# Kernel tuning notes

Hardware: AMD Instinct MI355X
Metric: run time of the kernel (lower is better)

## Reference

```python
import jax, jax.numpy as jnp
import numpy as np

B, N, M, C = 4, 4096, 4096, 256
IMG_W, IMG_H = 1242.0, 376.0  # KITTI-like image extents for keypoint coords


def setup_inputs() -> dict:
    key = jax.random.key(0)
    ks = jax.random.split(key, 12)
    s = 1.0 / np.sqrt(C)
    scale_uv = jnp.array([IMG_W, IMG_H], dtype=jnp.float32)
    return {
        "nodes_L": jax.random.normal(ks[0], (B, N, C), jnp.float32),
        "nodes_R": jax.random.normal(ks[1], (B, M, C), jnp.float32),
        "kpts_L": jax.random.uniform(ks[2], (B, N, 2), jnp.float32) * scale_uv,
        "kpts_R": jax.random.uniform(ks[3], (B, M, 2), jnp.float32) * scale_uv,
        "Wq": jax.random.normal(ks[4], (C, C), jnp.float32) * s,
        "bq": jnp.zeros((C,), jnp.float32),
        "Wk": jax.random.normal(ks[5], (C, C), jnp.float32) * s,
        "bk": jnp.zeros((C,), jnp.float32),
        "Wv": jax.random.normal(ks[6], (C, C), jnp.float32) * s,
        "bv": jnp.zeros((C,), jnp.float32),
        "Wm": jax.random.normal(ks[7], (C, C), jnp.float32) * s,
        "bm": jnp.zeros((C,), jnp.float32),
    }


def reference(nodes_L, nodes_R, kpts_L, kpts_R, Wq, bq, Wk, bk, Wv, bv, Wm, bm):
    dim = nodes_L.shape[-1]
    # torch.nn.Linear: y = x @ W.T + b  (W is [out, in])
    Q = jnp.einsum('bnc,dc->bnd', nodes_L, Wq) + bq  # [B,N,C]
    K = jnp.einsum('bmc,dc->bmd', nodes_R, Wk) + bk  # [B,M,C]
    V = jnp.einsum('bmc,dc->bmd', nodes_R, Wv) + bv  # [B,M,C]

    # Epipolar geometric mask from keypoint coordinates
    dist_v = jnp.abs(kpts_L[:, :, 1:2] - kpts_R[:, None, :, 1])  # [B,N,M]
    dist_u = kpts_L[:, :, 0:1] - kpts_R[:, None, :, 0]           # [B,N,M]
    mask = (dist_v < 3.0) & (dist_u > 0) & (dist_u < 192)

    attn = jnp.einsum('bnd,bmd->bnm', Q, K) / (dim ** 0.5)       # [B,N,M]
    attn = jnp.where(mask, attn, jnp.float32(-1e9))
    attn_weights = jax.nn.softmax(attn, axis=-1)                 # [B,N,M]

    matched_features = jnp.einsum('bnm,bmd->bnd', attn_weights, V)
    init_disparity = jnp.sum(attn_weights * dist_u, axis=-1, keepdims=True)  # [B,N,1]
    confidence = jnp.any(mask, axis=-1, keepdims=True).astype(jnp.float32)   # [B,N,1]
    out = jnp.einsum('bnd,cd->bnc', matched_features, Wm) + bm   # [B,N,C]
    return (out, init_disparity, confidence, attn_weights)
```

## Files before the change

### kernel.cpp

```cpp
#include <hip/hip_runtime.h>
#include <stdint.h>

#define CAP 192

typedef __attribute__((ext_vector_type(4))) float f32x4;
typedef __attribute__((ext_vector_type(8))) short bf16x8;

__device__ __forceinline__ float bf2f(ushort u) {
  return __uint_as_float(((unsigned)u) << 16);
}
__device__ __forceinline__ ushort f2bf(float f) {
  unsigned u = __float_as_uint(f);
  return (ushort)((u + 0x7fffu + ((u >> 16) & 1u)) >> 16);
}
__device__ __forceinline__ float wredsum(float v) {
#pragma unroll
  for (int o = 32; o; o >>= 1) v += __shfl_xor(v, o);
  return v;
}

__global__ __launch_bounds__(256) void prep(const float* __restrict__ nodesR,
                                            const float* __restrict__ kptsR,
                                            float* __restrict__ S16,
                                            float* __restrict__ sumU16,
                                            float* __restrict__ attn) {
  int t = threadIdx.x;
  if (blockIdx.x < 64) {
    int b = blockIdx.x >> 4, ch = blockIdx.x & 15;
    int c4 = (t & 63) * 4;
    int r0 = b * 4096 + ch * 256 + (t >> 6);
    float4 acc = {0.f, 0.f, 0.f, 0.f};
    for (int k = 0; k < 64; ++k) {
      float4 v = *(const float4*)(nodesR + (size_t)(r0 + k * 4) * 256 + c4);
      acc.x += v.x; acc.y += v.y; acc.z += v.z; acc.w += v.w;
    }
    __shared__ float4 red[256];
    red[t] = acc;
    float u = kptsR[(size_t)(b * 4096 + ch * 256 + t) * 2];
    u = wredsum(u);
    __shared__ float ured[4];
    if ((t & 63) == 0) ured[t >> 6] = u;
    __syncthreads();
    if (t < 64) {
      float4 x = red[t], y = red[t + 64], z = red[t + 128], w = red[t + 192];
      float4 s = { x.x + y.x + z.x + w.x, x.y + y.y + z.y + w.y,
                   x.z + y.z + z.z + w.z, x.w + y.w + z.w + w.w };
      *(float4*)(S16 + (size_t)(b * 16 + ch) * 256 + t * 4) = s;
    }
    if (t == 0) sumU16[b * 16 + ch] = ured[0] + ured[1] + ured[2] + ured[3];
  }
  f32x4 z = {0.f, 0.f, 0.f, 0.f};
  f32x4* dst = (f32x4*)attn;
  int g = blockIdx.x * 256 + t;
#pragma unroll
  for (int i = 0; i < 32; ++i)
    __builtin_nontemporal_store(z, dst + (size_t)g + (size_t)i * 524288);
}

template <bool A_BF16, typename OutT>
__device__ __forceinline__ void gemm_body(const void* __restrict__ Av,
                                          const float* __restrict__ Wf,
                                          const float* __restrict__ bias,
                                          OutT* __restrict__ Y, int blk,
                                          ushort* As, ushort* Bs) {
  int tid = threadIdx.x;
  int lane = tid & 63, wid = tid >> 6;
  int bm = blk >> 1, bn = blk & 1;
  int r0 = bm * 128, c0 = bn * 128;
  int wr = wid >> 1, wc = wid & 1;
  f32x4 acc[4][4] = {};
  for (int k0 = 0; k0 < 256; k0 += 32) {
    __syncthreads();
#pragma unroll
    for (int p = 0; p < 2; ++p) {
      int u = p * 2048 + tid * 8;
      int row = u >> 5, col = u & 31;
      if constexpr (A_BF16) {
        *(bf16x8*)&As[u] =
            *(const bf16x8*)((const ushort*)Av + (size_t)(r0 + row) * 256 + k0 + col);
      } else {
        const float* Af = (const float*)Av;
        float4 lo = *(const float4*)(Af + (size_t)(r0 + row) * 256 + k0 + col);
        float4 hi = *(const float4*)(Af + (size_t)(r0 + row) * 256 + k0 + col + 4);
        ushort4 o0 = { f2bf(lo.x), f2bf(lo.y), f2bf(lo.z), f2bf(lo.w) };
        ushort4 o1 = { f2bf(hi.x), f2bf(hi.y), f2bf(hi.z), f2bf(hi.w) };
        *(ushort4*)&As[u] = o0;
        *(ushort4*)&As[u + 4] = o1;
      }
      {
        float4 lo = *(const float4*)(Wf + (size_t)(c0 + row) * 256 + k0 + col);
        float4 hi = *(const float4*)(Wf + (size_t)(c0 + row) * 256 + k0 + col + 4);
        ushort4 o0 = { f2bf(lo.x), f2bf(lo.y), f2bf(lo.z), f2bf(lo.w) };
        ushort4 o1 = { f2bf(hi.x), f2bf(hi.y), f2bf(hi.z), f2bf(hi.w) };
        *(ushort4*)&Bs[u] = o0;
        *(ushort4*)&Bs[u + 4] = o1;
      }
    }
    __syncthreads();
    bf16x8 af[4], bfr[4];
    int rsel = lane & 15, ksel = (lane >> 4) * 8;
#pragma unroll
    for (int m = 0; m < 4; ++m)
      af[m] = *(bf16x8*)&As[(wr * 64 + m * 16 + rsel) * 32 + ksel];
#pragma unroll
    for (int n = 0; n < 4; ++n)
      bfr[n] = *(bf16x8*)&Bs[(wc * 64 + n * 16 + rsel) * 32 + ksel];
#pragma unroll
    for (int m = 0; m < 4; ++m)
#pragma unroll
      for (int n = 0; n < 4; ++n)
        acc[m][n] = __builtin_amdgcn_mfma_f32_16x16x32_bf16(af[m], bfr[n], acc[m][n], 0, 0, 0);
  }
  int rbase = r0 + wr * 64 + ((lane >> 4) * 4);
  int cbase = c0 + wc * 64 + (lane & 15);
#pragma unroll
  for (int n = 0; n < 4; ++n) {
    float bv = bias[cbase + n * 16];
#pragma unroll
    for (int m = 0; m < 4; ++m) {
#pragma unroll
      for (int j = 0; j < 4; ++j) {
        float v = acc[m][n][j] + bv;
        size_t idx = (size_t)(rbase + m * 16 + j) * 256 + (cbase + n * 16);
        if constexpr (sizeof(OutT) == 2) Y[idx] = (OutT)f2bf(v);
        else Y[idx] = (OutT)v;
      }
    }
  }
}

__global__ __launch_bounds__(256, 2) void gemm3p(
    const float* __restrict__ nodesL, const float* __restrict__ nodesR,
    const float* __restrict__ Wq, const float* __restrict__ Wk,
    const float* __restrict__ Wv, const float* __restrict__ bq,
    const float* __restrict__ bk, const float* __restrict__ bv,
    ushort* __restrict__ Qb, ushort* __restrict__ Kb, ushort* __restrict__ Vb,
    const float* __restrict__ S16, const float* __restrict__ sumU16,
    ushort* __restrict__ meanVb, float* __restrict__ meanU) {
  __shared__ __align__(16) ushort As[128 * 32];
  __shared__ __align__(16) ushort Bs[128 * 32];
  if (blockIdx.x == 768) {
    int c = threadIdx.x;
    float* sf = (float*)As;
    for (int b = 0; b < 4; ++b) {
      float a0 = 0.f;
      for (int ch = 0; ch < 16; ++ch) a0 += S16[(size_t)(b * 16 + ch) * 256 + c];
      sf[c] = a0;
      __syncthreads();
      float acc = 0.f;
      for (int k = 0; k < 256; k += 4) {
        float4 w = *(const float4*)(Wv + (size_t)c * 256 + k);
        acc += sf[k] * w.x + sf[k + 1] * w.y + sf[k + 2] * w.z + sf[k + 3] * w.w;
      }
      float mv = acc * (1.f / 4096.f) + bv[c];
      meanVb[b * 256 + c] = f2bf(mv);
      if (c == 0) {
        float su = 0.f;
        for (int ch = 0; ch < 16; ++ch) su += sumU16[b * 16 + ch];
        meanU[b] = su * (1.f / 4096.f);
      }
      __syncthreads();
    }
    return;
  }
  int which = blockIdx.x >> 8;
  int blk = blockIdx.x & 255;
  const float* A = (which == 0) ? nodesL : nodesR;
  const float* W = (which == 0) ? Wq : (which == 1) ? Wk : Wv;
  const float* bias = (which == 0) ? bq : (which == 1) ? bk : bv;
  ushort* Y = (which == 0) ? Qb : (which == 1) ? Kb : Vb;
  gemm_body<false, ushort>(A, W, bias, Y, blk, As, Bs);
}

__global__ __launch_bounds__(256, 2) void gemm_out(const ushort* __restrict__ A,
                                                   const float* __restrict__ Wm,
                                                   const float* __restrict__ bias,
                                                   float* __restrict__ Y) {
  __shared__ __align__(16) ushort As[128 * 32];
  __shared__ __align__(16) ushort Bs[128 * 32];
  gemm_body<true, float>(A, Wm, bias, Y, blockIdx.x, As, Bs);
}

__global__ __launch_bounds__(512, 2) void attn_fused(
    const float* __restrict__ kptsL, const float* __restrict__ kptsR,
    const ushort* __restrict__ Qb, const ushort* __restrict__ Kb,
    const ushort* __restrict__ Vb, const float* __restrict__ meanU,
    const ushort* __restrict__ meanVb, float* __restrict__ disp_out,
    float* __restrict__ conf_out, ushort* __restrict__ matched,
    float* __restrict__ attn) {
  __shared__ float2 kR[4096];
  __shared__ int bufM[8][CAP];
  __shared__ float bufD[8][CAP];
  __shared__ float bufS[8][CAP];
  int tid = threadIdx.x, lane = tid & 63, wid = tid >> 6;
  int b = blockIdx.x >> 9;
  int n = ((blockIdx.x & 511) << 3) + wid;
  int row = (b << 12) + n;
  int bb = b << 12;
  float* rowp = attn + (size_t)row * 4096;

  const float2* kRsrc = (const float2*)kptsR + (size_t)bb;
  for (int i = tid; i < 4096; i += 512) kR[i] = kRsrc[i];
  __syncthreads();
  float2 kL = ((const float2*)kptsL)[(size_t)row];
  ushort4 qv = *(const ushort4*)(Qb + (size_t)row * 256 + lane * 4);
  float q0 = bf2f(qv.x), q1 = bf2f(qv.y), q2 = bf2f(qv.z), q3 = bf2f(qv.w);

  unsigned long long lmask = (1ull << lane) - 1ull;
  int cnt = 0;
#pragma unroll 4
  for (int m0 = 0; m0 < 4096; m0 += 64) {
    float2 kr = kR[m0 + lane];
    float dv = fabsf(kL.y - kr.y);
    float du = kL.x - kr.x;
    bool hit = (dv < 3.0f) && (du > 0.0f) && (du < 192.0f);
    unsigned long long bal = __ballot(hit);
    int pos = cnt + (int)__popcll(bal & lmask);
    if (hit && pos < CAP) { bufM[wid][pos] = m0 + lane; bufD[wid][pos] = du; }
    cnt += (int)__popcll(bal);
  }
  if (cnt > CAP) cnt = CAP;

  float conf, disp;
  if (cnt == 0) {
    conf = 0.f;
    disp = kL.x - meanU[b];
    ushort4 st = *(const ushort4*)(meanVb + b * 256 + lane * 4);
    *(ushort4*)(matched + (size_t)row * 256 + lane * 4) = st;
    const float fill = 1.f / 4096.f;
    f32x4 fv = { fill, fill, fill, fill };
    f32x4* dst = (f32x4*)rowp;
#pragma unroll
    for (int j = 0; j < 16; ++j)
      __builtin_nontemporal_store(fv, dst + j * 64 + lane);
  } else {
    float mx = -1e30f;
    int i = 0;
    for (; i + 3 < cnt; i += 4) {
      int m0_ = bufM[wid][i], m1_ = bufM[wid][i + 1];
      int m2_ = bufM[wid][i + 2], m3_ = bufM[wid][i + 3];
      ushort4 k0 = *(const ushort4*)(Kb + ((size_t)(bb + m0_)) * 256 + lane * 4);
      ushort4 k1 = *(const ushort4*)(Kb + ((size_t)(bb + m1_)) * 256 + lane * 4);
      ushort4 k2 = *(const ushort4*)(Kb + ((size_t)(bb + m2_)) * 256 + lane * 4);
      ushort4 k3 = *(const ushort4*)(Kb + ((size_t)(bb + m3_)) * 256 + lane * 4);
      float p0 = q0 * bf2f(k0.x) + q1 * bf2f(k0.y) + q2 * bf2f(k0.z) + q3 * bf2f(k0.w);
      float p1 = q0 * bf2f(k1.x) + q1 * bf2f(k1.y) + q2 * bf2f(k1.z) + q3 * bf2f(k1.w);
      float p2 = q0 * bf2f(k2.x) + q1 * bf2f(k2.y) + q2 * bf2f(k2.z) + q3 * bf2f(k2.w);
      float p3 = q0 * bf2f(k3.x) + q1 * bf2f(k3.y) + q2 * bf2f(k3.z) + q3 * bf2f(k3.w);
#pragma unroll
      for (int o = 32; o; o >>= 1) {
        p0 += __shfl_xor(p0, o);
        p1 += __shfl_xor(p1, o);
        p2 += __shfl_xor(p2, o);
        p3 += __shfl_xor(p3, o);
      }
      float s0 = p0 * 0.0625f, s1 = p1 * 0.0625f;
      float s2 = p2 * 0.0625f, s3 = p3 * 0.0625f;
      if (lane == 0) {
        bufS[wid][i] = s0; bufS[wid][i + 1] = s1;
        bufS[wid][i + 2] = s2; bufS[wid][i + 3] = s3;
      }
      mx = fmaxf(mx, fmaxf(fmaxf(s0, s1), fmaxf(s2, s3)));
    }
    for (; i < cnt; ++i) {
      int ma = bufM[wid][i];
      ushort4 ka = *(const ushort4*)(Kb + ((size_t)(bb + ma)) * 256 + lane * 4);
      float pa = q0 * bf2f(ka.x) + q1 * bf2f(ka.y) + q2 * bf2f(ka.z) + q3 * bf2f(ka.w);
      pa = wredsum(pa);
      float sa = pa * 0.0625f;
      if (lane == 0) bufS[wid][i] = sa;
      mx = fmaxf(mx, sa);
    }
    float psum = 0.f, pdisp = 0.f;
    for (int k = lane; k < cnt; k += 64) {
      float e = expf(bufS[wid][k] - mx);
      bufS[wid][k] = e;
      psum += e;
      pdisp += e * bufD[wid][k];
    }
    psum = wredsum(psum);
    pdisp = wredsum(pdisp);
    float inv = 1.f / psum;
    disp = pdisp * inv;
    conf = 1.f;
    for (int k = lane; k < cnt; k += 64) bufS[wid][k] *= inv;
    float a0 = 0.f, a1 = 0.f, a2 = 0.f, a3 = 0.f;
    i = 0;
    for (; i + 3 < cnt; i += 4) {
      float w0 = bufS[wid][i], w1 = bufS[wid][i + 1];
      float w2 = bufS[wid][i + 2], w3 = bufS[wid][i + 3];
      int m0_ = bufM[wid][i], m1_ = bufM[wid][i + 1];
      int m2_ = bufM[wid][i + 2], m3_ = bufM[wid][i + 3];
      ushort4 v0 = *(const ushort4*)(Vb + ((size_t)(bb + m0_)) * 256 + lane * 4);
      ushort4 v1 = *(const ushort4*)(Vb + ((size_t)(bb + m1_)) * 256 + lane * 4);
      ushort4 v2 = *(const ushort4*)(Vb + ((size_t)(bb + m2_)) * 256 + lane * 4);
      ushort4 v3 = *(const ushort4*)(Vb + ((size_t)(bb + m3_)) * 256 + lane * 4);
      a0 += w0 * bf2f(v0.x) + w1 * bf2f(v1.x) + w2 * bf2f(v2.x) + w3 * bf2f(v3.x);
      a1 += w0 * bf2f(v0.y) + w1 * bf2f(v1.y) + w2 * bf2f(v2.y) + w3 * bf2f(v3.y);
      a2 += w0 * bf2f(v0.z) + w1 * bf2f(v1.z) + w2 * bf2f(v2.z) + w3 * bf2f(v3.z);
      a3 += w0 * bf2f(v0.w) + w1 * bf2f(v1.w) + w2 * bf2f(v2.w) + w3 * bf2f(v3.w);
    }
    for (; i < cnt; ++i) {
      float wa = bufS[wid][i];
      int ma = bufM[wid][i];
      ushort4 va = *(const ushort4*)(Vb + ((size_t)(bb + ma)) * 256 + lane * 4);
      a0 += wa * bf2f(va.x); a1 += wa * bf2f(va.y);
      a2 += wa * bf2f(va.z); a3 += wa * bf2f(va.w);
    }
    ushort4 st = { f2bf(a0), f2bf(a1), f2bf(a2), f2bf(a3) };
    *(ushort4*)(matched + (size_t)row * 256 + lane * 4) = st;
    for (int k = lane; k < cnt; k += 64)
      rowp[bufM[wid][k]] = bufS[wid][k];
  }
  if (lane == 0) { disp_out[row] = disp; conf_out[row] = conf; }
}

extern "C" void kernel_launch(void* const* d_in, const int* in_sizes, int n_in,
                              void* d_out, int out_size, void* d_ws, size_t ws_size,
                              hipStream_t stream) {
  const float* nodes_L = (const float*)d_in[0];
  const float* nodes_R = (const float*)d_in[1];
  const float* kpts_L = (const float*)d_in[2];
  const float* kpts_R = (const float*)d_in[3];
  const float* Wq = (const float*)d_in[4];
  const float* bq = (const float*)d_in[5];
  const float* Wk = (const float*)d_in[6];
  const float* bk = (const float*)d_in[7];
  const float* Wv = (const float*)d_in[8];
  const float* bv = (const float*)d_in[9];
  const float* Wm = (const float*)d_in[10];
  const float* bm = (const float*)d_in[11];

  float* out = (float*)d_out;
  float* disp = out + 4194304;
  float* conf = disp + 16384;
  float* attn = conf + 16384;

  char* ws = (char*)d_ws;
  ushort* Qb = (ushort*)(ws + 0);
  ushort* Kb = (ushort*)(ws + 8388608);
  ushort* Vb = (ushort*)(ws + 16777216);
  ushort* matched = (ushort*)(ws + 25165824);
  float* S16 = (float*)(ws + 33554432);
  float* sumU16 = (float*)(ws + 33620224);
  float* meanU = (float*)(ws + 33620480);
  ushort* meanVb = (ushort*)(ws + 33620544);

  prep<<<2048, 256, 0, stream>>>(nodes_R, kpts_R, S16, sumU16, attn);
  gemm3p<<<769, 256, 0, stream>>>(nodes_L, nodes_R, Wq, Wk, Wv, bq, bk, bv,
                                  Qb, Kb, Vb, S16, sumU16, meanVb, meanU);
  attn_fused<<<2048, 512, 0, stream>>>(kpts_L, kpts_R, Qb, Kb, Vb, meanU, meanVb,
                                       disp, conf, matched, attn);
  gemm_out<<<256, 256, 0, stream>>>(matched, Wm, bm, out);
}
```

Before: 474.4 us.

## Fuse all stages into one persistent cooperative kernel with grid syncs

Replaces the four separate launches (prep, QKV GEMM, attention, output GEMM) with a single cooperative kernel of 1024 blocks that uses grid-wide syncs between phases. The prep reduction and attention zero-fill move into the first phase, and each attention block now handles 16 rows with 4 rows per wave. The precomputed mean-V is replaced by an on-demand computation in rows with no epipolar match. The match buffer CAP shrinks from 192 to 128. This removes launch gaps and inter-kernel idle tails, at the cost of lower parallelism in the attention phase, grid-sync overhead, and a possible correctness change if a row has more than 128 matches.

Measured after the change: 791.8 us. +66.9%, slower.

```diff
diff --git a/kernel.cpp b/kernel.cpp
--- a/kernel.cpp
+++ b/kernel.cpp
@@ -1,7 +1,10 @@
 #include <hip/hip_runtime.h>
+#include <hip/hip_cooperative_groups.h>
 #include <stdint.h>
 
-#define CAP 192
+namespace cg = cooperative_groups;
+
+#define CAP 128
 
 typedef __attribute__((ext_vector_type(4))) float f32x4;
 typedef __attribute__((ext_vector_type(8))) short bf16x8;
@@ -17,44 +20,6 @@
 #pragma unroll
   for (int o = 32; o; o >>= 1) v += __shfl_xor(v, o);
   return v;
-}
-
-__global__ __launch_bounds__(256) void prep(const float* __restrict__ nodesR,
-                                            const float* __restrict__ kptsR,
-                                            float* __restrict__ S16,
-                                            float* __restrict__ sumU16,
-                                            float* __restrict__ attn) {
-  int t = threadIdx.x;
-  if (blockIdx.x < 64) {
-    int b = blockIdx.x >> 4, ch = blockIdx.x & 15;
-    int c4 = (t & 63) * 4;
-    int r0 = b * 4096 + ch * 256 + (t >> 6);
-    float4 acc = {0.f, 0.f, 0.f, 0.f};
-    for (int k = 0; k < 64; ++k) {
-      float4 v = *(const float4*)(nodesR + (size_t)(r0 + k * 4) * 256 + c4);
-      acc.x += v.x; acc.y += v.y; acc.z += v.z; acc.w += v.w;
-    }
-    __shared__ float4 red[256];
-    red[t] = acc;
-    float u = kptsR[(size_t)(b * 4096 + ch * 256 + t) * 2];
-    u = wredsum(u);
-    __shared__ float ured[4];
-    if ((t & 63) == 0) ured[t >> 6] = u;
-    __syncthreads();
-    if (t < 64) {
-      float4 x = red[t], y = red[t + 64], z = red[t + 128], w = red[t + 192];
-      float4 s = { x.x + y.x + z.x + w.x, x.y + y.y + z.y + w.y,
-                   x.z + y.z + z.z + w.z, x.w + y.w + z.w + w.w };
-      *(float4*)(S16 + (size_t)(b * 16 + ch) * 256 + t * 4) = s;
-    }
-    if (t == 0) sumU16[b * 16 + ch] = ured[0] + ured[1] + ured[2] + ured[3];
-  }
-  f32x4 z = {0.f, 0.f, 0.f, 0.f};
-  f32x4* dst = (f32x4*)attn;
-  int g = blockIdx.x * 256 + t;
-#pragma unroll
-  for (int i = 0; i < 32; ++i)
-    __builtin_nontemporal_store(z, dst + (size_t)g + (size_t)i * 524288);
 }
 
 template <bool A_BF16, typename OutT>
@@ -129,190 +94,238 @@
   }
 }
 
-__global__ __launch_bounds__(256, 2) void gemm3p(
+__device__ __forceinline__ void phase1_body(
     const float* __restrict__ nodesL, const float* __restrict__ nodesR,
-    const float* __restrict__ Wq, const float* __restrict__ Wk,
-    const float* __restrict__ Wv, const float* __restrict__ bq,
-    const float* __restrict__ bk, const float* __restrict__ bv,
+    const float* __restrict__ kptsR,
+    const float* __restrict__ Wq, const float* __restrict__ bq,
+    const float* __restrict__ Wk, const float* __restrict__ bk,
+    const float* __restrict__ Wv, const float* __restrict__ bv,
     ushort* __restrict__ Qb, ushort* __restrict__ Kb, ushort* __restrict__ Vb,
-    const float* __restrict__ S16, const float* __restrict__ sumU16,
-    ushort* __restrict__ meanVb, float* __restrict__ meanU) {
-  __shared__ __align__(16) ushort As[128 * 32];
-  __shared__ __align__(16) ushort Bs[128 * 32];
-  if (blockIdx.x == 768) {
-    int c = threadIdx.x;
-    float* sf = (float*)As;
-    for (int b = 0; b < 4; ++b) {
-      float a0 = 0.f;
-      for (int ch = 0; ch < 16; ++ch) a0 += S16[(size_t)(b * 16 + ch) * 256 + c];
-      sf[c] = a0;
-      __syncthreads();
-      float acc = 0.f;
-      for (int k = 0; k < 256; k += 4) {
-        float4 w = *(const float4*)(Wv + (size_t)c * 256 + k);
-        acc += sf[k] * w.x + sf[k + 1] * w.y + sf[k + 2] * w.z + sf[k + 3] * w.w;
-      }
-      float mv = acc * (1.f / 4096.f) + bv[c];
-      meanVb[b * 256 + c] = f2bf(mv);
-      if (c == 0) {
-        float su = 0.f;
-        for (int ch = 0; ch < 16; ++ch) su += sumU16[b * 16 + ch];
-        meanU[b] = su * (1.f / 4096.f);
-      }
-      __syncthreads();
-    }
-    return;
-  }
-  int which = blockIdx.x >> 8;
-  int blk = blockIdx.x & 255;
-  const float* A = (which == 0) ? nodesL : nodesR;
-  const float* W = (which == 0) ? Wq : (which == 1) ? Wk : Wv;
-  const float* bias = (which == 0) ? bq : (which == 1) ? bk : bv;
-  ushort* Y = (which == 0) ? Qb : (which == 1) ? Kb : Vb;
-  gemm_body<false, ushort>(A, W, bias, Y, blk, As, Bs);
-}
-
-__global__ __launch_bounds__(256, 2) void gemm_out(const ushort* __restrict__ A,
-                                                   const float* __restrict__ Wm,
-                                                   const float* __restrict__ bias,
-                                                   float* __restrict__ Y) {
-  __shared__ __align__(16) ushort As[128 * 32];
-  __shared__ __align__(16) ushort Bs[128 * 32];
-  gemm_body<true, float>(A, Wm, bias, Y, blockIdx.x, As, Bs);
-}
-
-__global__ __launch_bounds__(512, 2) void attn_fused(
+    float* __restrict__ S16, float* __restrict__ sumU16,
+    float* __restrict__ attn, char* smraw) {
+  int bid = blockIdx.x, tid = threadIdx.x;
+  ushort* As = (ushort*)smraw;
+  ushort* Bs = (ushort*)(smraw + 8192);
+  if (bid < 768) {
+    int which = bid >> 8, blk = bid & 255;
+    const float* A = (which == 0) ? nodesL : nodesR;
+    const float* W = (which == 0) ? Wq : (which == 1) ? Wk : Wv;
+    const float* bias = (which == 0) ? bq : (which == 1) ? bk : bv;
+    ushort* Y = (which == 0) ? Qb : (which == 1) ? Kb : Vb;
+    gemm_body<false, ushort>(A, W, bias, Y, blk, As, Bs);
+  } else if (bid < 832) {
+    int j = bid - 768;
+    int b = j >> 4, ch = j & 15;
+    int c4 = (tid & 63) * 4;
+    int r0 = b * 4096 + ch * 256 + (tid >> 6);
+    float4 acc = {0.f, 0.f, 0.f, 0.f};
+    for (int k = 0; k < 64; ++k) {
+      float4 v = *(const float4*)(nodesR + (size_t)(r0 + k * 4) * 256 + c4);
+      acc.x += v.x; acc.y += v.y; acc.z += v.z; acc.w += v.w;
+    }
+    float4* red = (float4*)As;
+    float* ured = (float*)Bs;
+    red[tid] = acc;
+    float u = kptsR[(size_t)(b * 4096 + ch * 256 + tid) * 2];
+    u = wredsum(u);
+    if ((tid & 63) == 0) ured[tid >> 6] = u;
+    __syncthreads();
+    if (tid < 64) {
+      float4 x = red[tid], y = red[tid + 64], z = red[tid + 128], w = red[tid + 192];
+      float4 s = { x.x + y.x + z.x + w.x, x.y + y.y + z.y + w.y,
+                   x.z + y.z + z.z + w.z, x.w + y.w + z.w + w.w };
+      *(float4*)(S16 + (size_t)(b * 16 + ch) * 256 + tid * 4) = s;
+    }
+    if (tid == 0) sumU16[b * 16 + ch] = ured[0] + ured[1] + ured[2] + ured[3];
+  }
+  f32x4 z = {0.f, 0.f, 0.f, 0.f};
+  f32x4* dst = (f32x4*)attn;
+  int g = bid * 256 + tid;
+#pragma unroll
+  for (int i = 0; i < 64; ++i)
+    __builtin_nontemporal_store(z, dst + (size_t)g + (size_t)i * 262144);
+}
+
+__device__ __forceinline__ void phase2_body(
     const float* __restrict__ kptsL, const float* __restrict__ kptsR,
     const ushort* __restrict__ Qb, const ushort* __restrict__ Kb,
-    const ushort* __restrict__ Vb, const float* __restrict__ meanU,
-    const ushort* __restrict__ meanVb, float* __restrict__ disp_out,
+    const ushort* __restrict__ Vb, const float* __restrict__ Wv,
+    const float* __restrict__ bv, const float* __restrict__ S16,
+    const float* __restrict__ sumU16, float* __restrict__ disp_out,
     float* __restrict__ conf_out, ushort* __restrict__ matched,
-    float* __restrict__ attn) {
-  __shared__ float2 kR[4096];
-  __shared__ int bufM[8][CAP];
-  __shared__ float bufD[8][CAP];
-  __shared__ float bufS[8][CAP];
-  int tid = threadIdx.x, lane = tid & 63, wid = tid >> 6;
-  int b = blockIdx.x >> 9;
-  int n = ((blockIdx.x & 511) << 3) + wid;
-  int row = (b << 12) + n;
+    float* __restrict__ attn, char* smraw) {
+  float2* kR = (float2*)smraw;
+  int   (*bufM)[CAP] = (int(*)[CAP])(smraw + 32768);
+  float (*bufD)[CAP] = (float(*)[CAP])(smraw + 34816);
+  float (*bufS)[CAP] = (float(*)[CAP])(smraw + 36864);
+  int bid = blockIdx.x, tid = threadIdx.x;
+  int lane = tid & 63, wid = tid >> 6;
+  int b = bid >> 8;
   int bb = b << 12;
-  float* rowp = attn + (size_t)row * 4096;
-
   const float2* kRsrc = (const float2*)kptsR + (size_t)bb;
-  for (int i = tid; i < 4096; i += 512) kR[i] = kRsrc[i];
+  for (int i = tid; i < 4096; i += 256) kR[i] = kRsrc[i];
   __syncthreads();
-  float2 kL = ((const float2*)kptsL)[(size_t)row];
-  ushort4 qv = *(const ushort4*)(Qb + (size_t)row * 256 + lane * 4);
-  float q0 = bf2f(qv.x), q1 = bf2f(qv.y), q2 = bf2f(qv.z), q3 = bf2f(qv.w);
-
   unsigned long long lmask = (1ull << lane) - 1ull;
-  int cnt = 0;
+
+  for (int r = 0; r < 4; ++r) {
+    int row = bid * 16 + wid * 4 + r;
+    float* rowp = attn + (size_t)row * 4096;
+    float2 kL = ((const float2*)kptsL)[(size_t)row];
+    ushort4 qv = *(const ushort4*)(Qb + (size_t)row * 256 + lane * 4);
+    float q0 = bf2f(qv.x), q1 = bf2f(qv.y), q2 = bf2f(qv.z), q3 = bf2f(qv.w);
+
+    int cnt = 0;
 #pragma unroll 4
-  for (int m0 = 0; m0 < 4096; m0 += 64) {
-    float2 kr = kR[m0 + lane];
-    float dv = fabsf(kL.y - kr.y);
-    float du = kL.x - kr.x;
-    bool hit = (dv < 3.0f) && (du > 0.0f) && (du < 192.0f);
-    unsigned long long bal = __ballot(hit);
-    int pos = cnt + (int)__popcll(bal & lmask);
-    if (hit && pos < CAP) { bufM[wid][pos] = m0 + lane; bufD[wid][pos] = du; }
-    cnt += (int)__popcll(bal);
-  }
-  if (cnt > CAP) cnt = CAP;
-
-  float conf, disp;
-  if (cnt == 0) {
-    conf = 0.f;
-    disp = kL.x - meanU[b];
-    ushort4 st = *(const ushort4*)(meanVb + b * 256 + lane * 4);
-    *(ushort4*)(matched + (size_t)row * 256 + lane * 4) = st;
-    const float fill = 1.f / 4096.f;
-    f32x4 fv = { fill, fill, fill, fill };
-    f32x4* dst = (f32x4*)rowp;
-#pragma unroll
-    for (int j = 0; j < 16; ++j)
-      __builtin_nontemporal_store(fv, dst + j * 64 + lane);
-  } else {
-    float mx = -1e30f;
-    int i = 0;
-    for (; i + 3 < cnt; i += 4) {
-      int m0_ = bufM[wid][i], m1_ = bufM[wid][i + 1];
-      int m2_ = bufM[wid][i + 2], m3_ = bufM[wid][i + 3];
-      ushort4 k0 = *(const ushort4*)(Kb + ((size_t)(bb + m0_)) * 256 + lane * 4);
-      ushort4 k1 = *(const ushort4*)(Kb + ((size_t)(bb + m1_)) * 256 + lane * 4);
-      ushort4 k2 = *(const ushort4*)(Kb + ((size_t)(bb + m2_)) * 256 + lane * 4);
-      ushort4 k3 = *(const ushort4*)(Kb + ((size_t)(bb + m3_)) * 256 + lane * 4);
-      float p0 = q0 * bf2f(k0.x) + q1 * bf2f(k0.y) + q2 * bf2f(k0.z) + q3 * bf2f(k0.w);
-      float p1 = q0 * bf2f(k1.x) + q1 * bf2f(k1.y) + q2 * bf2f(k1.z) + q3 * bf2f(k1.w);
-      float p2 = q0 * bf2f(k2.x) + q1 * bf2f(k2.y) + q2 * bf2f(k2.z) + q3 * bf2f(k2.w);
-      float p3 = q0 * bf2f(k3.x) + q1 * bf2f(k3.y) + q2 * bf2f(k3.z) + q3 * bf2f(k3.w);
-#pragma unroll
-      for (int o = 32; o; o >>= 1) {
-        p0 += __shfl_xor(p0, o);
-        p1 += __shfl_xor(p1, o);
-        p2 += __shfl_xor(p2, o);
-        p3 += __shfl_xor(p3, o);
-      }
-      float s0 = p0 * 0.0625f, s1 = p1 * 0.0625f;
-      float s2 = p2 * 0.0625f, s3 = p3 * 0.0625f;
-      if (lane == 0) {
-        bufS[wid][i] = s0; bufS[wid][i + 1] = s1;
-        bufS[wid][i + 2] = s2; bufS[wid][i + 3] = s3;
-      }
-      mx = fmaxf(mx, fmaxf(fmaxf(s0, s1), fmaxf(s2, s3)));
-    }
-    for (; i < cnt; ++i) {
-      int ma = bufM[wid][i];
-      ushort4 ka = *(const ushort4*)(Kb + ((size_t)(bb + ma)) * 256 + lane * 4);
-      float pa = q0 * bf2f(ka.x) + q1 * bf2f(ka.y) + q2 * bf2f(ka.z) + q3 * bf2f(ka.w);
-      pa = wredsum(pa);
-      float sa = pa * 0.0625f;
-      if (lane == 0) bufS[wid][i] = sa;
-      mx = fmaxf(mx, sa);
-    }
-    float psum = 0.f, pdisp = 0.f;
-    for (int k = lane; k < cnt; k += 64) {
-      float e = expf(bufS[wid][k] - mx);
-      bufS[wid][k] = e;
-      psum += e;
-      pdisp += e * bufD[wid][k];
-    }
-    psum = wredsum(psum);
-    pdisp = wredsum(pdisp);
-    float inv = 1.f / psum;
-    disp = pdisp * inv;
-    conf = 1.f;
-    for (int k = lane; k < cnt; k += 64) bufS[wid][k] *= inv;
-    float a0 = 0.f, a1 = 0.f, a2 = 0.f, a3 = 0.f;
-    i = 0;
-    for (; i + 3 < cnt; i += 4) {
-      float w0 = bufS[wid][i], w1 = bufS[wid][i + 1];
-      float w2 = bufS[wid][i + 2], w3 = bufS[wid][i + 3];
-      int m0_ = bufM[wid][i], m1_ = bufM[wid][i + 1];
-      int m2_ = bufM[wid][i + 2], m3_ = bufM[wid][i + 3];
-      ushort4 v0 = *(const ushort4*)(Vb + ((size_t)(bb + m0_)) * 256 + lane * 4);
-      ushort4 v1 = *(const ushort4*)(Vb + ((size_t)(bb + m1_)) * 256 + lane * 4);
-      ushort4 v2 = *(const ushort4*)(Vb + ((size_t)(bb + m2_)) * 256 + lane * 4);
-      ushort4 v3 = *(const ushort4*)(Vb + ((size_t)(bb + m3_)) * 256 + lane * 4);
-      a0 += w0 * bf2f(v0.x) + w1 * bf2f(v1.x) + w2 * bf2f(v2.x) + w3 * bf2f(v3.x);
-      a1 += w0 * bf2f(v0.y) + w1 * bf2f(v1.y) + w2 * bf2f(v2.y) + w3 * bf2f(v3.y);
-      a2 += w0 * bf2f(v0.z) + w1 * bf2f(v1.z) + w2 * bf2f(v2.z) + w3 * bf2f(v3.z);
-      a3 += w0 * bf2f(v0.w) + w1 * bf2f(v1.w) + w2 * bf2f(v2.w) + w3 * bf2f(v3.w);
-    }
-    for (; i < cnt; ++i) {
-      float wa = bufS[wid][i];
-      int ma = bufM[wid][i];
-      ushort4 va = *(const ushort4*)(Vb + ((size_t)(bb + ma)) * 256 + lane * 4);
-      a0 += wa * bf2f(va.x); a1 += wa * bf2f(va.y);
-      a2 += wa * bf2f(va.z); a3 += wa * bf2f(va.w);
-    }
-    ushort4 st = { f2bf(a0), f2bf(a1), f2bf(a2), f2bf(a3) };
-    *(ushort4*)(matched + (size_t)row * 256 + lane * 4) = st;
-    for (int k = lane; k < cnt; k += 64)
-      rowp[bufM[wid][k]] = bufS[wid][k];
-  }
-  if (lane == 0) { disp_out[row] = disp; conf_out[row] = conf; }
+    for (int m0 = 0; m0 < 4096; m0 += 64) {
+      float2 kr = kR[m0 + lane];
+      float dv = fabsf(kL.y - kr.y);
+      float du = kL.x - kr.x;
+      bool hit = (dv < 3.0f) && (du > 0.0f) && (du < 192.0f);
+      unsigned long long bal = __ballot(hit);
+      int pos = cnt + (int)__popcll(bal & lmask);
+      if (hit && pos < CAP) { bufM[wid][pos] = m0 + lane; bufD[wid][pos] = du; }
+      cnt += (int)__popcll(bal);
+    }
+    if (cnt > CAP) cnt = CAP;
+
+    float conf, disp;
+    if (cnt == 0) {
+      conf = 0.f;
+      float su = 0.f;
+      for (int ch = 0; ch < 16; ++ch) su += sumU16[b * 16 + ch];
+      disp = kL.x - su * (1.f / 4096.f);
+      for (int k = lane; k < 256; k += 64) {
+        float s = 0.f;
+        for (int ch = 0; ch < 16; ++ch) s += S16[(size_t)(b * 16 + ch) * 256 + k];
+        if (k < 128) bufD[wid][k] = s; else bufS[wid][k - 128] = s;
+      }
+      float mv[4];
+#pragma unroll
+      for (int j = 0; j < 4; ++j) {
+        int c = lane * 4 + j;
+        float acc = 0.f;
+        for (int k = 0; k < 256; ++k) {
+          float sv = (k < 128) ? bufD[wid][k] : bufS[wid][k - 128];
+          acc += sv * Wv[(size_t)c * 256 + k];
+        }
+        mv[j] = acc * (1.f / 4096.f) + bv[c];
+      }
+      ushort4 st = { f2bf(mv[0]), f2bf(mv[1]), f2bf(mv[2]), f2bf(mv[3]) };
+      *(ushort4*)(matched + (size_t)row * 256 + lane * 4) = st;
+      const float fill = 1.f / 4096.f;
+      f32x4 fv = { fill, fill, fill, fill };
+      f32x4* dstp = (f32x4*)rowp;
+#pragma unroll
+      for (int jj = 0; jj < 16; ++jj)
+        __builtin_nontemporal_store(fv, dstp + jj * 64 + lane);
+    } else {
+      float mx = -1e30f;
+      int i = 0;
+      for (; i + 3 < cnt; i += 4) {
+        int m0_ = bufM[wid][i], m1_ = bufM[wid][i + 1];
+        int m2_ = bufM[wid][i + 2], m3_ = bufM[wid][i + 3];
+        ushort4 k0 = *(const ushort4*)(Kb + ((size_t)(bb + m0_)) * 256 + lane * 4);
+        ushort4 k1 = *(const ushort4*)(Kb + ((size_t)(bb + m1_)) * 256 + lane * 4);
+        ushort4 k2 = *(const ushort4*)(Kb + ((size_t)(bb + m2_)) * 256 + lane * 4);
+        ushort4 k3 = *(const ushort4*)(Kb + ((size_t)(bb + m3_)) * 256 + lane * 4);
+        float p0 = q0 * bf2f(k0.x) + q1 * bf2f(k0.y) + q2 * bf2f(k0.z) + q3 * bf2f(k0.w);
+        float p1 = q0 * bf2f(k1.x) + q1 * bf2f(k1.y) + q2 * bf2f(k1.z) + q3 * bf2f(k1.w);
+        float p2 = q0 * bf2f(k2.x) + q1 * bf2f(k2.y) + q2 * bf2f(k2.z) + q3 * bf2f(k2.w);
+        float p3 = q0 * bf2f(k3.x) + q1 * bf2f(k3.y) + q2 * bf2f(k3.z) + q3 * bf2f(k3.w);
+#pragma unroll
+        for (int o = 32; o; o >>= 1) {
+          p0 += __shfl_xor(p0, o);
+          p1 += __shfl_xor(p1, o);
+          p2 += __shfl_xor(p2, o);
+          p3 += __shfl_xor(p3, o);
+        }
+        float s0 = p0 * 0.0625f, s1 = p1 * 0.0625f;
+        float s2 = p2 * 0.0625f, s3 = p3 * 0.0625f;
+        if (lane == 0) {
+          bufS[wid][i] = s0; bufS[wid][i + 1] = s1;
+          bufS[wid][i + 2] = s2; bufS[wid][i + 3] = s3;
+        }
+        mx = fmaxf(mx, fmaxf(fmaxf(s0, s1), fmaxf(s2, s3)));
+      }
+      for (; i < cnt; ++i) {
+        int ma = bufM[wid][i];
+        ushort4 ka = *(const ushort4*)(Kb + ((size_t)(bb + ma)) * 256 + lane * 4);
+        float pa = q0 * bf2f(ka.x) + q1 * bf2f(ka.y) + q2 * bf2f(ka.z) + q3 * bf2f(ka.w);
+        pa = wredsum(pa);
+        float sa = pa * 0.0625f;
+        if (lane == 0) bufS[wid][i] = sa;
+        mx = fmaxf(mx, sa);
+      }
+      float psum = 0.f, pdisp = 0.f;
+      for (int k = lane; k < cnt; k += 64) {
+        float e = expf(bufS[wid][k] - mx);
+        bufS[wid][k] = e;
+        psum += e;
+        pdisp += e * bufD[wid][k];
+      }
+      psum = wredsum(psum);
+      pdisp = wredsum(pdisp);
+      float inv = 1.f / psum;
+      disp = pdisp * inv;
+      conf = 1.f;
+      for (int k = lane; k < cnt; k += 64) bufS[wid][k] *= inv;
+      float a0 = 0.f, a1 = 0.f, a2 = 0.f, a3 = 0.f;
+      i = 0;
+      for (; i + 3 < cnt; i += 4) {
+        float w0 = bufS[wid][i], w1 = bufS[wid][i + 1];
+        float w2 = bufS[wid][i + 2], w3 = bufS[wid][i + 3];
+        int m0_ = bufM[wid][i], m1_ = bufM[wid][i + 1];
+        int m2_ = bufM[wid][i + 2], m3_ = bufM[wid][i + 3];
+        ushort4 v0 = *(const ushort4*)(Vb + ((size_t)(bb + m0_)) * 256 + lane * 4);
+        ushort4 v1 = *(const ushort4*)(Vb + ((size_t)(bb + m1_)) * 256 + lane * 4);
+        ushort4 v2 = *(const ushort4*)(Vb + ((size_t)(bb + m2_)) * 256 + lane * 4);
+        ushort4 v3 = *(const ushort4*)(Vb + ((size_t)(bb + m3_)) * 256 + lane * 4);
+        a0 += w0 * bf2f(v0.x) + w1 * bf2f(v1.x) + w2 * bf2f(v2.x) + w3 * bf2f(v3.x);
+        a1 += w0 * bf2f(v0.y) + w1 * bf2f(v1.y) + w2 * bf2f(v2.y) + w3 * bf2f(v3.y);
+        a2 += w0 * bf2f(v0.z) + w1 * bf2f(v1.z) + w2 * bf2f(v2.z) + w3 * bf2f(v3.z);
+        a3 += w0 * bf2f(v0.w) + w1 * bf2f(v1.w) + w2 * bf2f(v2.w) + w3 * bf2f(v3.w);
+      }
+      for (; i < cnt; ++i) {
+        float wa = bufS[wid][i];
+        int ma = bufM[wid][i];
+        ushort4 va = *(const ushort4*)(Vb + ((size_t)(bb + ma)) * 256 + lane * 4);
+        a0 += wa * bf2f(va.x); a1 += wa * bf2f(va.y);
+        a2 += wa * bf2f(va.z); a3 += wa * bf2f(va.w);
+      }
+      ushort4 st = { f2bf(a0), f2bf(a1), f2bf(a2), f2bf(a3) };
+      *(ushort4*)(matched + (size_t)row * 256 + lane * 4) = st;
+      for (int k = lane; k < cnt; k += 64)
+        rowp[bufM[wid][k]] = bufS[wid][k];
+    }
+    if (lane == 0) { disp_out[row] = disp; conf_out[row] = conf; }
+  }
+}
+
+template <int PHASE>
+__global__ __launch_bounds__(256, 4) void mega(
+    const float* nodesL, const float* nodesR,
+    const float* kptsL, const float* kptsR,
+    const float* Wq, const float* bq, const float* Wk, const float* bk,
+    const float* Wv, const float* bv, const float* Wm, const float* bm,
+    ushort* Qb, ushort* Kb, ushort* Vb, ushort* matched,
+    float* S16, float* sumU16,
+    float* out, float* disp_out, float* conf_out, float* attn) {
+  __shared__ __align__(16) char smraw[38912];
+  if constexpr (PHASE == 0 || PHASE == 3)
+    phase1_body(nodesL, nodesR, kptsR, Wq, bq, Wk, bk, Wv, bv,
+                Qb, Kb, Vb, S16, sumU16, attn, smraw);
+  if constexpr (PHASE == 3) cg::this_grid().sync();
+  if constexpr (PHASE == 1 || PHASE == 3)
+    phase2_body(kptsL, kptsR, Qb, Kb, Vb, Wv, bv, S16, sumU16,
+                disp_out, conf_out, matched, attn, smraw);
+  if constexpr (PHASE == 3) cg::this_grid().sync();
+  if constexpr (PHASE == 2 || PHASE == 3) {
+    if (blockIdx.x < 256) {
+      ushort* As = (ushort*)smraw;
+      ushort* Bs = (ushort*)(smraw + 8192);
+      gemm_body<true, float>(matched, Wm, bm, out, blockIdx.x, As, Bs);
+    }
+  }
 }
 
 extern "C" void kernel_launch(void* const* d_in, const int* in_sizes, int n_in,
@@ -343,13 +356,26 @@
   ushort* matched = (ushort*)(ws + 25165824);
   float* S16 = (float*)(ws + 33554432);
   float* sumU16 = (float*)(ws + 33620224);
-  float* meanU = (float*)(ws + 33620480);
-  ushort* meanVb = (ushort*)(ws + 33620544);
-
-  prep<<<2048, 256, 0, stream>>>(nodes_R, kpts_R, S16, sumU16, attn);
-  gemm3p<<<769, 256, 0, stream>>>(nodes_L, nodes_R, Wq, Wk, Wv, bq, bk, bv,
-                                  Qb, Kb, Vb, S16, sumU16, meanVb, meanU);
-  attn_fused<<<2048, 512, 0, stream>>>(kpts_L, kpts_R, Qb, Kb, Vb, meanU, meanVb,
-                                       disp, conf, matched, attn);
-  gemm_out<<<256, 256, 0, stream>>>(matched, Wm, bm, out);
-}
+
+  void* args[] = {
+    (void*)&nodes_L, (void*)&nodes_R, (void*)&kpts_L, (void*)&kpts_R,
+    (void*)&Wq, (void*)&bq, (void*)&Wk, (void*)&bk,
+    (void*)&Wv, (void*)&bv, (void*)&Wm, (void*)&bm,
+    (void*)&Qb, (void*)&Kb, (void*)&Vb, (void*)&matched,
+    (void*)&S16, (void*)&sumU16,
+    (void*)&out, (void*)&disp, (void*)&conf, (void*)&attn
+  };
+  hipError_t e = hipLaunchCooperativeKernel(
+      reinterpret_cast<const void*>(&mega<3>), dim3(1024), dim3(256), args, 0, stream);
+  if (e != hipSuccess) {
+    mega<0><<<1024, 256, 0, stream>>>(nodes_L, nodes_R, kpts_L, kpts_R, Wq, bq, Wk, bk,
+                                      Wv, bv, Wm, bm, Qb, Kb, Vb, matched, S16, sumU16,
+                                      out, disp, conf, attn);
+    mega<1><<<1024, 256, 0, stream>>>(nodes_L, nodes_R, kpts_L, kpts_R, Wq, bq, Wk, bk,
+                                      Wv, bv, Wm, bm, Qb, Kb, Vb, matched, S16, sumU16,
+                                      out, disp, conf, attn);
+    mega<2><<<256, 256, 0, stream>>>(nodes_L, nodes_R, kpts_L, kpts_R, Wq, bq, Wk, bk,
+                                     Wv, bv, Wm, bm, Qb, Kb, Vb, matched, S16, sumU16,
+                                     out, disp, conf, attn);
+  }
+}
```
